# Performance work log

Measured on AMD Instinct MI355X. Metric: run time of the kernel, lower is better.

Reference implementation:

```python
import jax, jax.numpy as jnp
import numpy as np

LOW_T = 0.05
HIGH_T = 0.15

SOBEL_X = jnp.array([[-1., 0., 1.], [-2., 0., 2.], [-1., 0., 1.]], dtype=jnp.float32).reshape(1, 1, 3, 3)
SOBEL_Y = jnp.array([[1., 2., 1.], [0., 0., 0.], [-1., -2., -1.]], dtype=jnp.float32).reshape(1, 1, 3, 3)


def _conv3x3(x, k):
    # NCHW conv, padding=1, stride=1 (matches F.conv2d(x, k, padding=1))
    return jax.lax.conv_general_dilated(x, k, window_strides=(1, 1), padding=((1, 1), (1, 1)))


def setup_inputs() -> dict:
    key = jax.random.key(0)
    x = jax.random.normal(key, (1, 1, 4096, 4096), dtype=jnp.float32)
    return {"x": x}


def reference(x):
    grad_x = _conv3x3(x, SOBEL_X)
    grad_y = _conv3x3(x, SOBEL_Y)
    grad_mag = jnp.sqrt(grad_x * grad_x + grad_y * grad_y)
    grad_dir = jnp.arctan2(grad_y, grad_x)  # radians, as in the original (compared to degree thresholds)

    m = grad_mag[0, 0]  # [H, W]
    d = grad_dir[0, 0][1:-1, 1:-1]  # direction at interior pixels [H-2, W-2]
    H, W = m.shape

    def sh(dr, dc):
        # magnitude at (row+dr, col+dc) for interior pixels
        return m[1 + dr:H - 1 + dr, 1 + dc:W - 1 + dc]

    mc = sh(0, 0)

    # Branch predicates replicated literally from the torch code (degree thresholds
    # vs radian values; some sub-conditions are vacuously false, kept for faithfulness).
    b1 = ((d >= -22.5) & (d <= 22.5)) | ((d >= 157.5) & (d <= 180.0)) | ((d >= -157.5) & (d <= -180.0))
    b2 = ((d > 22.5) & (d <= 67.5)) | ((d >= -112.5) & (d < -157.5))
    b3 = ((d > 67.5) & (d <= 112.5)) | ((d >= -67.5) & (d < -22.5))

    mag_prev = jnp.where(b1, sh(0, -1), jnp.where(b2, sh(-1, 1), jnp.where(b3, sh(-1, 0), sh(-1, -1))))
    mag_next = jnp.where(b1, sh(0, 1), jnp.where(b2, sh(1, -1), jnp.where(b3, sh(1, 0), sh(1, 1))))

    keep = (mc >= mag_prev) & (mc >= mag_next)
    interior = jnp.where(keep, mc, jnp.zeros_like(mc))
    edges = jnp.zeros_like(m).at[1:-1, 1:-1].set(interior)

    # Double thresholding: strong -> 255, weak ([low, high]) -> 0, below-low passes through.
    strong = edges > HIGH_T
    weak = (edges >= LOW_T) & (edges <= HIGH_T)
    out = jnp.where(strong, jnp.float32(255.0), jnp.where(weak, jnp.float32(0.0), edges))
    return out  # [H, W]
```

## Files before the change

kernel.cpp:

```cpp
#include <hip/hip_runtime.h>
#include <math.h>


constexpr int Wd = 4096;
constexpr int Ht = 4096;
constexpr int TW = 64;
constexpr int TH = 32;
constexpr int LH  = TH + 2;
constexpr int LSC = 19;
constexpr int NCH = LH * LSC;

__global__ __launch_bounds__(256) void canny_kernel(const float* __restrict__ x,
                                                    float* __restrict__ out) {
    __shared__ float4 xs[NCH];
    const int tid = threadIdx.x;
    const int c0 = blockIdx.x * TW;
    const int r0 = blockIdx.y * TH;

    #pragma unroll
    for (int k = 0; k < 3; ++k) {
        int i = tid + k * 256;
        if (i < NCH) {
            int lr = i / LSC;
            int cc = i - lr * LSC;
            int r = r0 - 1 + lr;
            int c = c0 - 4 + 4 * cc;
            float4 v = make_float4(0.f, 0.f, 0.f, 0.f);
            if ((unsigned)r < (unsigned)Ht && (unsigned)c < (unsigned)Wd)
                v = *reinterpret_cast<const float4*>(x + (size_t)r * Wd + c);
            xs[i] = v;
        }
    }
    __syncthreads();

    const int rl  = tid >> 3;
    const int seg = tid & 7;
    const int r   = r0 + rl;
    const int cbase = c0 + seg * 8;

    const float4* pa = &xs[rl * LSC + seg * 2];
    const float4* pb = pa + LSC;
    const float4* pc = pa + 2 * LSC;

    float ar[16], br[16], cr[16];
    #pragma unroll
    for (int k = 0; k < 4; ++k) {
        *reinterpret_cast<float4*>(&ar[4 * k]) = pa[k];
        *reinterpret_cast<float4*>(&br[4 * k]) = pb[k];
        *reinterpret_cast<float4*>(&cr[4 * k]) = pc[k];
    }

    float t1[16], t2[16];
    #pragma unroll
    for (int j = 2; j < 14; ++j) {
        t1[j] = ar[j] + 2.0f * br[j] + cr[j];
        t2[j] = ar[j] - cr[j];
    }

    float m[10];
    #pragma unroll
    for (int s = 0; s < 10; ++s) {
        int j = s + 3;
        float gx = t1[j + 1] - t1[j - 1];
        float gy = t2[j - 1] + 2.0f * t2[j] + t2[j + 1];
        m[s] = sqrtf(gx * gx + gy * gy);
    }

    float acc[8];
    #pragma unroll
    for (int s = 0; s < 8; ++s) {
        float mc = m[s + 1];
        bool keep = (mc >= m[s]) && (mc >= m[s + 2]);
        float e = keep ? mc : 0.0f;
        acc[s] = (e > 0.15f) ? 255.0f : ((e >= 0.05f) ? 0.0f : e);
    }

    if (r == 0 || r == Ht - 1) {
        #pragma unroll
        for (int s = 0; s < 8; ++s) acc[s] = 0.0f;
    }
    if (cbase == 0)           acc[0] = 0.0f;
    if (cbase + 7 == Wd - 1)  acc[7] = 0.0f;

    float4* o4 = reinterpret_cast<float4*>(out + (size_t)r * Wd + cbase);
    o4[0] = make_float4(acc[0], acc[1], acc[2], acc[3]);
    o4[1] = make_float4(acc[4], acc[5], acc[6], acc[7]);
}

extern "C" void kernel_launch(void* const* d_in, const int* in_sizes, int n_in,
                              void* d_out, int out_size, void* d_ws, size_t ws_size,
                              hipStream_t stream) {
    const float* x = (const float*)d_in[0];
    float* out = (float*)d_out;
    dim3 grid(Wd / TW, Ht / TH);
    canny_kernel<<<grid, dim3(256), 0, stream>>>(x, out);
}
```

Before: 124.6 us.

## Drop LDS staging, load stencil rows directly from global with nontemporal stores

Removes the shared-memory tile and barrier. Each thread now loads its three input rows straight from global memory, relying on L1/L2 to absorb the overlapping reads between neighbouring threads and rows. The block layout changes to 64 strips of 8 columns by 4 rows, so a wavefront covers a contiguous 2KB row span. Output is written with nontemporal stores to keep it from polluting the cache. The cost is redundant global loads (3x rows plus overlapping halo float4s), which now depend on cache hit rates.

```diff
diff --git a/kernel.cpp b/kernel.cpp
--- a/kernel.cpp
+++ b/kernel.cpp
@@ -4,87 +4,75 @@
 
 constexpr int Wd = 4096;
 constexpr int Ht = 4096;
-constexpr int TW = 64;
-constexpr int TH = 32;
-constexpr int LH  = TH + 2;
-constexpr int LSC = 19;
-constexpr int NCH = LH * LSC;
+
+typedef float f4 __attribute__((ext_vector_type(4)));
 
 __global__ __launch_bounds__(256) void canny_kernel(const float* __restrict__ x,
                                                     float* __restrict__ out) {
-    __shared__ float4 xs[NCH];
-    const int tid = threadIdx.x;
-    const int c0 = blockIdx.x * TW;
-    const int r0 = blockIdx.y * TH;
+    const int tid   = threadIdx.x;
+    const int strip = blockIdx.x * 64 + (tid & 63);
+    const int r     = blockIdx.y * 4  + (tid >> 6);
+    const int cbase = strip * 8;
 
-    #pragma unroll
-    for (int k = 0; k < 3; ++k) {
-        int i = tid + k * 256;
-        if (i < NCH) {
-            int lr = i / LSC;
-            int cc = i - lr * LSC;
-            int r = r0 - 1 + lr;
-            int c = c0 - 4 + 4 * cc;
-            float4 v = make_float4(0.f, 0.f, 0.f, 0.f);
-            if ((unsigned)r < (unsigned)Ht && (unsigned)c < (unsigned)Wd)
-                v = *reinterpret_cast<const float4*>(x + (size_t)r * Wd + c);
-            xs[i] = v;
-        }
-    }
-    __syncthreads();
+    const int rm = (r == 0) ? 0 : r - 1;
+    const int rp = (r == Ht - 1) ? Ht - 1 : r + 1;
+    const bool left  = (cbase == 0);
+    const bool right = (cbase + 8 == Wd);
 
-    const int rl  = tid >> 3;
-    const int seg = tid & 7;
-    const int r   = r0 + rl;
-    const int cbase = c0 + seg * 8;
-
-    const float4* pa = &xs[rl * LSC + seg * 2];
-    const float4* pb = pa + LSC;
-    const float4* pc = pa + 2 * LSC;
+    const float* xa = x + (size_t)rm * Wd + (cbase - 4);
+    const float* xb = x + (size_t)r  * Wd + (cbase - 4);
+    const float* xc = x + (size_t)rp * Wd + (cbase - 4);
 
     float ar[16], br[16], cr[16];
+    const f4 z4 = {0.f, 0.f, 0.f, 0.f};
     #pragma unroll
     for (int k = 0; k < 4; ++k) {
-        *reinterpret_cast<float4*>(&ar[4 * k]) = pa[k];
-        *reinterpret_cast<float4*>(&br[4 * k]) = pb[k];
-        *reinterpret_cast<float4*>(&cr[4 * k]) = pc[k];
+        const bool ok = !((k == 0 && left) || (k == 3 && right));
+        f4 va = ok ? *reinterpret_cast<const f4*>(xa + 4 * k) : z4;
+        f4 vb = ok ? *reinterpret_cast<const f4*>(xb + 4 * k) : z4;
+        f4 vc = ok ? *reinterpret_cast<const f4*>(xc + 4 * k) : z4;
+        *reinterpret_cast<f4*>(&ar[4 * k]) = va;
+        *reinterpret_cast<f4*>(&br[4 * k]) = vb;
+        *reinterpret_cast<f4*>(&cr[4 * k]) = vc;
     }
 
-    float t1[16], t2[16];
+    float t1[12], t2[12];
     #pragma unroll
-    for (int j = 2; j < 14; ++j) {
-        t1[j] = ar[j] + 2.0f * br[j] + cr[j];
-        t2[j] = ar[j] - cr[j];
+    for (int i = 0; i < 12; ++i) {
+        float a = ar[i + 2], b = br[i + 2], c = cr[i + 2];
+        t1[i] = a + 2.0f * b + c;
+        t2[i] = a - c;
     }
 
     float m[10];
     #pragma unroll
     for (int s = 0; s < 10; ++s) {
-        int j = s + 3;
-        float gx = t1[j + 1] - t1[j - 1];
-        float gy = t2[j - 1] + 2.0f * t2[j] + t2[j + 1];
+        float gx = t1[s + 2] - t1[s];
+        float gy = t2[s] + 2.0f * t2[s + 1] + t2[s + 2];
         m[s] = sqrtf(gx * gx + gy * gy);
     }
 
     float acc[8];
     #pragma unroll
-    for (int s = 0; s < 8; ++s) {
-        float mc = m[s + 1];
-        bool keep = (mc >= m[s]) && (mc >= m[s + 2]);
+    for (int o = 0; o < 8; ++o) {
+        float mc = m[o + 1];
+        bool keep = (mc >= m[o]) && (mc >= m[o + 2]);
         float e = keep ? mc : 0.0f;
-        acc[s] = (e > 0.15f) ? 255.0f : ((e >= 0.05f) ? 0.0f : e);
+        acc[o] = (e > 0.15f) ? 255.0f : ((e >= 0.05f) ? 0.0f : e);
     }
 
     if (r == 0 || r == Ht - 1) {
         #pragma unroll
-        for (int s = 0; s < 8; ++s) acc[s] = 0.0f;
+        for (int o = 0; o < 8; ++o) acc[o] = 0.0f;
     }
-    if (cbase == 0)           acc[0] = 0.0f;
-    if (cbase + 7 == Wd - 1)  acc[7] = 0.0f;
+    if (left)  acc[0] = 0.0f;
+    if (right) acc[7] = 0.0f;
 
-    float4* o4 = reinterpret_cast<float4*>(out + (size_t)r * Wd + cbase);
-    o4[0] = make_float4(acc[0], acc[1], acc[2], acc[3]);
-    o4[1] = make_float4(acc[4], acc[5], acc[6], acc[7]);
+    float* op = out + (size_t)r * Wd + cbase;
+    f4 lo = {acc[0], acc[1], acc[2], acc[3]};
+    f4 hi = {acc[4], acc[5], acc[6], acc[7]};
+    __builtin_nontemporal_store(lo, reinterpret_cast<f4*>(op));
+    __builtin_nontemporal_store(hi, reinterpret_cast<f4*>(op) + 1);
 }
 
 extern "C" void kernel_launch(void* const* d_in, const int* in_sizes, int n_in,
@@ -92,6 +80,6 @@
                               hipStream_t stream) {
     const float* x = (const float*)d_in[0];
     float* out = (float*)d_out;
-    dim3 grid(Wd / TW, Ht / TH);
+    dim3 grid(Wd / (64 * 8), Ht / 4);
     canny_kernel<<<grid, dim3(256), 0, stream>>>(x, out);
 }
```

New measurement: 114.4 us. 1.09x faster.
